# Kernel tuning notes

Measured on AMD Instinct MI355X. Metric: run time of the kernel, lower is better.

## Reference

```python
import jax, jax.numpy as jnp
import numpy as np

CUR, FULL, BS, D = 1024, 2048, 4, 1024
HN, HD = 16, 64
PREV = FULL - CUR
SCALE = 1.0 / HD ** 0.5


def rel_shift(x):
    # x: (bs, hn, cur, full) -> TXL relative shift over last two dims
    b, h, q, k = x.shape
    x = jnp.pad(x, ((0, 0), (0, 0), (0, 0), (1, 0)))  # (b,h,q,k+1)
    x = x.reshape(b, h, k + 1, q)[:, :, 1:, :]
    return x.reshape(b, h, q, k)


def setup_inputs() -> dict:
    key = jax.random.key(0)
    ks = jax.random.split(key, 16)
    s = 0.02
    inputs = jax.random.normal(ks[0], (CUR, BS, D), jnp.float32)
    pos_embedding = jax.random.normal(ks[1], (FULL, 1, D), jnp.float32)
    full_input = jax.random.normal(ks[2], (FULL, BS, D), jnp.float32)
    # causal mask: query i (absolute pos i+PREV) cannot attend to key j > i+PREV
    i = jnp.arange(CUR)[:, None]
    j = jnp.arange(FULL)[None, :]
    mask = (j > i + PREV)[:, :, None]  # (cur, full, 1) bool
    W_kv = jax.random.normal(ks[3], (D, 2 * HN * HD), jnp.float32) * s
    b_kv = jnp.zeros((2 * HN * HD,), jnp.float32)
    W_q = jax.random.normal(ks[4], (D, HN * HD), jnp.float32) * s
    b_q = jnp.zeros((HN * HD,), jnp.float32)
    W_pos = jax.random.normal(ks[5], (D, HN * HD), jnp.float32) * s
    b_pos = jnp.zeros((HN * HD,), jnp.float32)
    W_proj = jax.random.normal(ks[6], (HN * HD, D), jnp.float32) * s
    b_proj = jnp.zeros((D,), jnp.float32)
    u = jax.random.normal(ks[7], (HN, HD), jnp.float32) * s
    v = jax.random.normal(ks[8], (HN, HD), jnp.float32) * s
    return dict(inputs=inputs, pos_embedding=pos_embedding, full_input=full_input,
                u=u, v=v, mask=mask, W_kv=W_kv, b_kv=b_kv, W_q=W_q, b_q=b_q,
                W_pos=W_pos, b_pos=b_pos, W_proj=W_proj, b_proj=b_proj)


def reference(inputs, pos_embedding, full_input, u, v, mask,
              W_kv, b_kv, W_q, b_q, W_pos, b_pos, W_proj, b_proj):
    cur, bs, _ = inputs.shape
    full = full_input.shape[0]
    kv = full_input @ W_kv + b_kv                      # (full, bs, 2*hn*hd)
    k, val = jnp.split(kv, 2, axis=-1)
    k = k.reshape(full, bs, HN, HD)
    val = val.reshape(full, bs, HN, HD)
    q = (inputs @ W_q + b_q).reshape(cur, bs, HN, HD)
    r = (pos_embedding @ W_pos + b_pos).reshape(full, HN, HD)
    content = jnp.einsum('ibhd,jbhd->bhij', q + u, k)   # (bs,hn,cur,full)
    position = jnp.einsum('ibhd,jhd->bhij', q + v, r)
    position = rel_shift(position)
    attn = (content + position) * SCALE
    attn = jnp.where(mask[None, :, :, 0][:, None, :, :], -jnp.inf, attn)
    attn = jax.nn.softmax(attn, axis=-1)
    out = jnp.einsum('bhij,jbhd->ibhd', attn, val).reshape(cur, bs, HN * HD)
    return out @ W_proj + b_proj
```

## Files before the change

### kernel.cpp

```cpp
#include <hip/hip_runtime.h>


typedef _Float16 half8 __attribute__((ext_vector_type(8)));
typedef _Float16 half4v __attribute__((ext_vector_type(4)));
typedef float f32x4 __attribute__((ext_vector_type(4)));

typedef const __attribute__((address_space(1))) void* gas_ptr;
typedef __attribute__((address_space(3))) void* las_ptr;

__device__ __forceinline__ void load_lds16(const void* g, void* l) {
  __builtin_amdgcn_global_load_lds((gas_ptr)g, (las_ptr)l, 16, 0, 0);
}

__global__ __launch_bounds__(256) void prep(
    const float* __restrict__ inputs, const float* __restrict__ full_inp,
    const float* __restrict__ pos_emb, const float* __restrict__ Wq,
    const float* __restrict__ Wkv, const float* __restrict__ Wpos,
    const float* __restrict__ Wproj, _Float16* __restrict__ o_in,
    _Float16* __restrict__ o_full, _Float16* __restrict__ o_pos,
    _Float16* __restrict__ owq, _Float16* __restrict__ owkv,
    _Float16* __restrict__ owpos, _Float16* __restrict__ owproj) {
  __shared__ _Float16 tile[64][65];
  const int bx = blockIdx.x;
  const int t = threadIdx.x;
  if (bx < 2048) {
#pragma unroll
    for (int it = 0; it < 7; ++it) {
      const size_t g = (size_t)bx * 256 + t + (size_t)it * (2048 * 256);
      float4 vv;
      _Float16* dptr;
      if (g < (1u << 20)) {
        const int rd = (int)(g >> 8), b = rd >> 10, i = rd & 1023;
        const size_t sg = ((size_t)(i * 4 + b) << 8) + (g & 255);
        vv = *(const float4*)(inputs + sg * 4);
        dptr = o_in + g * 4;
      } else if (g < (3u << 20)) {
        const size_t gd = g - (1u << 20);
        const int rd = (int)(gd >> 8), b = rd >> 11, j = rd & 2047;
        const size_t sg = ((size_t)(j * 4 + b) << 8) + (gd & 255);
        vv = *(const float4*)(full_inp + sg * 4);
        dptr = o_full + gd * 4;
      } else {
        const size_t gd = g - (3u << 20);
        vv = *(const float4*)(pos_emb + gd * 4);
        dptr = o_pos + gd * 4;
      }
      half4v hh;
      hh[0] = (_Float16)vv.x; hh[1] = (_Float16)vv.y;
      hh[2] = (_Float16)vv.z; hh[3] = (_Float16)vv.w;
      *(half4v*)dptr = hh;
    }
    return;
  }
  const int wb = bx - 2048;
  const float* W;
  _Float16* Wt;
  int N, tidx;
  if (wb < 256) { W = Wq; Wt = owq; N = 1024; tidx = wb; }
  else if (wb < 768) { W = Wkv; Wt = owkv; N = 2048; tidx = wb - 256; }
  else if (wb < 1024) { W = Wpos; Wt = owpos; N = 1024; tidx = wb - 768; }
  else { W = Wproj; Wt = owproj; N = 1024; tidx = wb - 1024; }
  const int K = 1024;
  const int n0 = (tidx % (N >> 6)) * 64, k0 = (tidx / (N >> 6)) * 64;
  const int rr = t >> 2, cc = (t & 3) * 16;
#pragma unroll
  for (int i = 0; i < 4; ++i) {
    float4 v = *(const float4*)&W[(size_t)(k0 + rr) * N + n0 + cc + i * 4];
    tile[rr][cc + i * 4 + 0] = (_Float16)v.x;
    tile[rr][cc + i * 4 + 1] = (_Float16)v.y;
    tile[rr][cc + i * 4 + 2] = (_Float16)v.z;
    tile[rr][cc + i * 4 + 3] = (_Float16)v.w;
  }
  __syncthreads();
  const int n = t >> 2, kc = (t & 3) * 16;
#pragma unroll
  for (int i = 0; i < 4; ++i) {
    half4v h;
    h[0] = tile[kc + i * 4 + 0][n];
    h[1] = tile[kc + i * 4 + 1][n];
    h[2] = tile[kc + i * 4 + 2][n];
    h[3] = tile[kc + i * 4 + 3][n];
    *(half4v*)&Wt[(size_t)(n0 + n) * K + k0 + kc + i * 4] = h;
  }
}

__global__ __launch_bounds__(256, 2) void gemm3(
    const _Float16* __restrict__ Aq, const _Float16* __restrict__ Akv,
    const _Float16* __restrict__ Ar, const _Float16* __restrict__ Btq,
    const _Float16* __restrict__ Btkv, const _Float16* __restrict__ Btr,
    const float* __restrict__ bq, const float* __restrict__ bkv,
    const float* __restrict__ br, const float* __restrict__ uu,
    _Float16* __restrict__ qfu, _Float16* __restrict__ kf,
    _Float16* __restrict__ vfT, _Float16* __restrict__ rf) {
  __shared__ _Float16 smem[128 * 128];
  _Float16* As = smem;
  _Float16* Bs = smem + 8192;
  const int gb = blockIdx.x;
  const _Float16* A;
  const _Float16* Bt;
  const float* bias;
  int mode, bm, bn;
  if (gb < 256) {
    mode = 1; A = Aq; Bt = Btq; bias = bq;
    bn = (gb & 7) * 128; bm = (gb >> 3) * 128;
  } else if (gb < 1280) {
    mode = 2; A = Akv; Bt = Btkv; bias = bkv;
    const int j = gb - 256;
    bn = (j & 15) * 128; bm = (j >> 4) * 128;
  } else {
    mode = 3; A = Ar; Bt = Btr; bias = br;
    const int j = gb - 1280;
    bn = (j & 7) * 128; bm = (j >> 3) * 128;
  }
  const int K = 1024;
  const int t = threadIdx.x, w = t >> 6, l = t & 63;
  const int l15 = l & 15, l4 = l >> 4;
  const int wm = (w >> 1) * 64, wn = (w & 1) * 64;

  f32x4 acc[4][4];
  const f32x4 z4 = {0.f, 0.f, 0.f, 0.f};
#pragma unroll
  for (int i = 0; i < 4; ++i)
#pragma unroll
    for (int j = 0; j < 4; ++j) acc[i][j] = z4;

  const char* Abase = (const char*)A + (size_t)bm * K * 2;
  const char* Bbase = (const char*)Bt + (size_t)bn * K * 2;

  for (int k0 = 0; k0 < K; k0 += 64) {
    __syncthreads();
#pragma unroll
    for (int iss = 0; iss < 4; ++iss) {
      const int off = w * 4096 + iss * 1024 + l * 16;
      const int row = off >> 7;
      const int sw = ((((off >> 4) & 7) ^ (row & 7)) << 4);
      load_lds16(Abase + (size_t)row * (K * 2) + k0 * 2 + sw, (char*)As + off);
      load_lds16(Bbase + (size_t)row * (K * 2) + k0 * 2 + sw, (char*)Bs + off);
    }
    __syncthreads();
#pragma unroll
    for (int ks = 0; ks < 2; ++ks) {
      const int ch = ((ks * 4 + l4) ^ (l15 & 7)) * 8;
      half8 af[4], bf[4];
#pragma unroll
      for (int mt = 0; mt < 4; ++mt)
        af[mt] = *(const half8*)&As[(wm + mt * 16 + l15) * 64 + ch];
#pragma unroll
      for (int nt = 0; nt < 4; ++nt)
        bf[nt] = *(const half8*)&Bs[(wn + nt * 16 + l15) * 64 + ch];
#pragma unroll
      for (int mt = 0; mt < 4; ++mt)
#pragma unroll
        for (int nt = 0; nt < 4; ++nt)
          acc[mt][nt] = __builtin_amdgcn_mfma_f32_16x16x32_f16(
              af[mt], bf[nt], acc[mt][nt], 0, 0, 0);
    }
  }

  if (mode == 2 && bn >= 1024) {
    const int b = bm >> 11, j0m = bm & 2047;
    const int hbase = (bn - 1024) >> 6;
#pragma unroll
    for (int ch = 0; ch < 2; ++ch) {
      __syncthreads();
      if (((wn >> 6) & 1) == ch) {
#pragma unroll
        for (int mt = 0; mt < 4; ++mt)
#pragma unroll
          for (int r = 0; r < 4; ++r) {
            const int rowl = wm + mt * 16 + l4 * 4 + r;
#pragma unroll
            for (int nt = 0; nt < 4; ++nt) {
              const int coll = nt * 16 + l15;
              smem[rowl * 66 + coll] =
                  (_Float16)(acc[mt][nt][r] + bias[bn + wn + coll]);
            }
          }
      }
      __syncthreads();
#pragma unroll
      for (int it = 0; it < 4; ++it) {
        const int c = t + 256 * it;
        const int d = c >> 4, ck = c & 15;
        half8 v8;
#pragma unroll
        for (int z = 0; z < 8; ++z) v8[z] = smem[(ck * 8 + z) * 66 + d];
        *(half8*)&vfT[(((size_t)(b * 16 + hbase + ch) * 64 + d) << 11) + j0m +
                      ck * 8] = v8;
      }
    }
    return;
  }

#pragma unroll
  for (int mt = 0; mt < 4; ++mt)
#pragma unroll
    for (int r = 0; r < 4; ++r) {
      const int rowl = wm + mt * 16 + l4 * 4 + r;
#pragma unroll
      for (int nt = 0; nt < 4; ++nt) {
        const int col = bn + wn + nt * 16 + l15;
        const float val = acc[mt][nt][r] + bias[col];
        if (mode == 1) {
          const int b = bm >> 10, i0m = bm & 1023;
          const int h = col >> 6, d = col & 63;
          qfu[(((size_t)(b * 16 + h) * 1024 + i0m + rowl) << 6) + d] =
              (_Float16)((val + uu[col]) * 0.125f);
        } else if (mode == 2) {
          const int b = bm >> 11, j0m = bm & 2047;
          const int h = col >> 6, d = col & 63;
          kf[(((size_t)(b * 16 + h) * 2048 + j0m + rowl) << 6) + d] =
              (_Float16)val;
        } else {
          const int h = col >> 6, d = col & 63;
          rf[(((size_t)h * 2048 + bm + rowl) << 6) + d] = (_Float16)val;
        }
      }
    }
}

__global__ __launch_bounds__(256, 2) void gemm_proj(
    const _Float16* __restrict__ A, const _Float16* __restrict__ Bt,
    const float* __restrict__ bias, float* __restrict__ out0, int M, int N,
    int K) {
  __shared__ _Float16 As[128 * 64];
  __shared__ _Float16 Bs[64 * 64];
  const int t = threadIdx.x, w = t >> 6, l = t & 63;
  const int l15 = l & 15, l4 = l >> 4;
  const int bm = blockIdx.y * 128, bn = blockIdx.x * 64;
  const int wm = (w >> 1) * 64, wn = (w & 1) * 32;

  f32x4 acc[4][2];
  const f32x4 z4 = {0.f, 0.f, 0.f, 0.f};
#pragma unroll
  for (int i = 0; i < 4; ++i)
#pragma unroll
    for (int j = 0; j < 2; ++j) acc[i][j] = z4;

  const char* Abase = (const char*)A + (size_t)bm * K * 2;
  const char* Bbase = (const char*)Bt + (size_t)bn * K * 2;

  for (int k0 = 0; k0 < K; k0 += 64) {
    __syncthreads();
#pragma unroll
    for (int iss = 0; iss < 4; ++iss) {
      const int off = w * 4096 + iss * 1024 + l * 16;
      const int row = off >> 7;
      const int sw = ((((off >> 4) & 7) ^ (row & 7)) << 4);
      load_lds16(Abase + (size_t)row * (K * 2) + k0 * 2 + sw, (char*)As + off);
    }
#pragma unroll
    for (int iss = 0; iss < 2; ++iss) {
      const int off = w * 1024 + iss * 4096 + l * 16;
      const int row = off >> 7;
      const int sw = ((((off >> 4) & 7) ^ (row & 7)) << 4);
      load_lds16(Bbase + (size_t)row * (K * 2) + k0 * 2 + sw, (char*)Bs + off);
    }
    __syncthreads();
#pragma unroll
    for (int ks = 0; ks < 2; ++ks) {
      const int ch = ((ks * 4 + l4) ^ (l15 & 7)) * 8;
      half8 af[4], bf[2];
#pragma unroll
      for (int mt = 0; mt < 4; ++mt)
        af[mt] = *(const half8*)&As[(wm + mt * 16 + l15) * 64 + ch];
#pragma unroll
      for (int nt = 0; nt < 2; ++nt)
        bf[nt] = *(const half8*)&Bs[(wn + nt * 16 + l15) * 64 + ch];
#pragma unroll
      for (int mt = 0; mt < 4; ++mt)
#pragma unroll
        for (int nt = 0; nt < 2; ++nt)
          acc[mt][nt] = __builtin_amdgcn_mfma_f32_16x16x32_f16(
              af[mt], bf[nt], acc[mt][nt], 0, 0, 0);
    }
  }

#pragma unroll
  for (int mt = 0; mt < 4; ++mt)
#pragma unroll
    for (int r = 0; r < 4; ++r) {
      const int row = bm + wm + mt * 16 + l4 * 4 + r;
#pragma unroll
      for (int nt = 0; nt < 2; ++nt) {
        const int col = bn + wn + nt * 16 + l15;
        out0[(size_t)row * N + col] = acc[mt][nt][r] + bias[col];
      }
    }
}

__global__ __launch_bounds__(256, 2) void attn_mfma(
    const _Float16* __restrict__ qfu,
    const _Float16* __restrict__ kf,
    const _Float16* __restrict__ vfT,
    const _Float16* __restrict__ rf,
    const float* __restrict__ u,
    const float* __restrict__ v,
    _Float16* __restrict__ attn_out)
{
  __shared__ _Float16 ks[64 * 64];
  __shared__ _Float16 vts[64 * 64];
  __shared__ _Float16 rs[256 * 64];
  __shared__ _Float16 pA[2][4][16 * 64];

  const int t = threadIdx.x, w = t >> 6, l = t & 63;
  const int l15 = l & 15, l4 = l >> 4;
  const int id = blockIdx.x;
  const int bh = ((id >> 3) & 7) * 8 + (id & 7);
  const int qt = id >> 6;
  const int bx = (qt < 4) ? (7 - qt) : (qt - 4);
  const int i0 = bx * 128;
  const int h = bh & 15, b = bh >> 4;

  const char* kfb = (const char*)(kf + (((size_t)bh * 2048) << 6));
  const char* vg = (const char*)(vfT + (((size_t)bh) << 17));
  const char* rg = (const char*)(rf + (((size_t)h) << 17));

  half8 qa0[2], qa1[2], qv0[2], qv1[2];
  {
    half8 dl0, dl1;
#pragma unroll
    for (int z = 0; z < 8; ++z) {
      const int di = l4 * 8 + z;
      dl0[z] = (_Float16)(0.125f * (v[h * 64 + di] - u[h * 64 + di]));
      dl1[z] = (_Float16)(0.125f * (v[h * 64 + 32 + di] - u[h * 64 + 32 + di]));
    }
#pragma unroll
    for (int g = 0; g < 2; ++g) {
      const size_t qo =
          (((size_t)bh * 1024 + i0 + 64 * g + w * 16 + l15) << 6) + l4 * 8;
      qa0[g] = *(const half8*)(qfu + qo);
      qa1[g] = *(const half8*)(qfu + qo + 32);
      qv0[g] = qa0[g] + dl0;
      qv1[g] = qa1[g] + dl1;
    }
  }
  const f32x4 z4 = {0.f, 0.f, 0.f, 0.f};
  f32x4 o[2][4];
  float lsum[2][4];
#pragma unroll
  for (int g = 0; g < 2; ++g)
#pragma unroll
    for (int nt = 0; nt < 4; ++nt) { o[g][nt] = z4; lsum[g][nt] = 0.f; }

  const int mb0 = 960 - i0;
  const int njt = 2 * bx + 18;

#pragma unroll
  for (int iss = 0; iss < 6; ++iss) {
    const int off = w * 1024 + iss * 4096 + l * 16;
    const int q = off >> 7;
    const int cph = (off >> 4) & 7;
    const int slot = (mb0 - 64 + q) & 255;
    int m = mb0 - 64 + q;
    m = m < 2047 ? m : 2047;
    load_lds16(rg + (size_t)m * 128 + ((cph ^ (slot & 7)) << 4),
               (char*)rs + slot * 128 + cph * 16);
  }

  for (int jt = 0; jt < njt; ++jt) {
    const int j0 = jt * 64;
    const int m_base = j0 - i0 + 960;
    __syncthreads();
    {
      const char* kg = kfb + (size_t)j0 * 128;
#pragma unroll
      for (int iss = 0; iss < 2; ++iss) {
        const int off = w * 1024 + iss * 4096 + l * 16;
        const int row = off >> 7;
        const int cph = (off >> 4) & 7;
        const int sw = ((cph ^ (row & 7)) << 4);
        load_lds16(kg + (size_t)row * 128 + sw, (char*)ks + off);
        load_lds16(vg + (size_t)row * 4096 + (size_t)j0 * 2 + sw,
                   (char*)vts + off);
      }
    }
    if (jt > 0) {
      const int m0 = m_base + 64;
#pragma unroll
      for (int iss = 0; iss < 2; ++iss) {
        const int off = w * 1024 + iss * 4096 + l * 16;
        const int q = off >> 7;
        const int cph = (off >> 4) & 7;
        const int slot = (m0 + q) & 255;
        int m = m0 + q;
        m = m < 2047 ? m : 2047;
        load_lds16(rg + (size_t)m * 128 + ((cph ^ (slot & 7)) << 4),
                   (char*)rs + slot * 128 + cph * 16);
      }
    }
    __syncthreads();

    f32x4 sc[2][4];
    __builtin_amdgcn_s_setprio(1);
#pragma unroll
    for (int nt = 0; nt < 4; ++nt) {
      const int row = nt * 16 + l15;
      const int rsw = row & 7;
      const half8 b0 = *(const half8*)&ks[row * 64 + ((l4 ^ rsw) * 8)];
      const half8 b1 = *(const half8*)&ks[row * 64 + (((4 + l4) ^ rsw) * 8)];
#pragma unroll
      for (int g = 0; g < 2; ++g) {
        f32x4 cc = z4;
        cc = __builtin_amdgcn_mfma_f32_16x16x32_f16(qa0[g], b0, cc, 0, 0, 0);
        cc = __builtin_amdgcn_mfma_f32_16x16x32_f16(qa1[g], b1, cc, 0, 0, 0);
        sc[g][nt] = cc;
      }
    }
    __builtin_amdgcn_s_setprio(0);

#pragma unroll
    for (int g = 0; g < 2; ++g) {
      const int cw = i0 + 64 * g - j0 + 1024 + 16 * w;
      if (g == 0 && cw < -15) continue;
      const int mbg = m_base - 64 * g;
      f32x4 accP[5];
      __builtin_amdgcn_s_setprio(1);
#pragma unroll
      for (int p = 0; p < 5; ++p) {
        const int m = mbg + (3 - w + p) * 16 + l15;
        const int slot = m & 255;
        const int ssw = slot & 7;
        const half8 b0 = *(const half8*)&rs[slot * 64 + ((l4 ^ ssw) * 8)];
        const half8 b1 = *(const half8*)&rs[slot * 64 + (((4 + l4) ^ ssw) * 8)];
        f32x4 cc = z4;
        cc = __builtin_amdgcn_mfma_f32_16x16x32_f16(qv0[g], b0, cc, 0, 0, 0);
        cc = __builtin_amdgcn_mfma_f32_16x16x32_f16(qv1[g], b1, cc, 0, 0, 0);
        accP[p] = cc;
      }
      __builtin_amdgcn_s_setprio(0);
      if (cw >= 63) {
#pragma unroll
        for (int r = 0; r < 4; ++r) {
          const int thr = 4 * l4 + r;
          const int srcl = (l4 << 4) | ((15 + l15 - thr) & 15);
          float rot[5];
#pragma unroll
          for (int p = 0; p < 5; ++p) rot[p] = __shfl(accP[p][r], srcl, 64);
          float esum = 0.f;
          const int sw2 = (thr & 7) * 8;
#pragma unroll
          for (int nt = 0; nt < 4; ++nt) {
            const float pv = (l15 <= thr) ? rot[nt] : rot[nt + 1];
            const float e = __expf(sc[g][nt][r] + pv);
            esum += e;
            pA[g][w][thr * 64 + ((16 * nt + l15) ^ sw2)] = (_Float16)e;
          }
          lsum[g][r] += esum;
        }
      } else {
#pragma unroll
        for (int r = 0; r < 4; ++r) {
          const int thr = 4 * l4 + r;
          const int srcl = (l4 << 4) | ((15 + l15 - thr) & 15);
          float rot[5];
#pragma unroll
          for (int p = 0; p < 5; ++p) rot[p] = __shfl(accP[p][r], srcl, 64);
          float esum = 0.f;
          const int sw2 = (thr & 7) * 8;
#pragma unroll
          for (int nt = 0; nt < 4; ++nt) {
            const float pv = (l15 <= thr) ? rot[nt] : rot[nt + 1];
            const bool masked = (16 * nt + l15) > (cw + thr);
            const float e = masked ? 0.f : __expf(sc[g][nt][r] + pv);
            esum += e;
            pA[g][w][thr * 64 + ((16 * nt + l15) ^ sw2)] = (_Float16)e;
          }
          lsum[g][r] += esum;
        }
      }
    }

    const bool act0 = (i0 - j0 + 1024 + 16 * w) >= -15;
    __builtin_amdgcn_s_setprio(1);
#pragma unroll
    for (int kk = 0; kk < 2; ++kk) {
      const int aoff = l15 * 64 + ((kk * 32 + l4 * 8) ^ ((l15 & 7) * 8));
      half8 a81 = *(const half8*)&pA[1][w][aoff];
      half8 a80;
      if (act0) a80 = *(const half8*)&pA[0][w][aoff];
#pragma unroll
      for (int nt = 0; nt < 4; ++nt) {
        const int row = nt * 16 + l15;
        const half8 b8 =
            *(const half8*)&vts[row * 64 + ((((kk << 2) + l4) ^ (row & 7)) * 8)];
        if (act0)
          o[0][nt] =
              __builtin_amdgcn_mfma_f32_16x16x32_f16(a80, b8, o[0][nt], 0, 0, 0);
        o[1][nt] =
            __builtin_amdgcn_mfma_f32_16x16x32_f16(a81, b8, o[1][nt], 0, 0, 0);
      }
    }
    __builtin_amdgcn_s_setprio(0);
  }

#pragma unroll
  for (int g = 0; g < 2; ++g)
#pragma unroll
    for (int r = 0; r < 4; ++r) {
      float s = lsum[g][r];
      s += __shfl_xor(s, 1, 64);
      s += __shfl_xor(s, 2, 64);
      s += __shfl_xor(s, 4, 64);
      s += __shfl_xor(s, 8, 64);
      const float inv = 1.0f / s;
      const int i = i0 + 64 * g + w * 16 + l4 * 4 + r;
      const size_t base = ((size_t)i * 4 + b) * 1024 + h * 64;
#pragma unroll
      for (int nt = 0; nt < 4; ++nt)
        attn_out[base + nt * 16 + l15] = (_Float16)(o[g][nt][r] * inv);
    }
}

extern "C" void kernel_launch(void* const* d_in, const int* in_sizes, int n_in,
                              void* d_out, int out_size, void* d_ws,
                              size_t ws_size, hipStream_t stream) {
  const float* inputs   = (const float*)d_in[0];
  const float* pos_emb  = (const float*)d_in[1];
  const float* full_inp = (const float*)d_in[2];
  const float* u        = (const float*)d_in[3];
  const float* v        = (const float*)d_in[4];
  const float* W_kv   = (const float*)d_in[6];
  const float* b_kv   = (const float*)d_in[7];
  const float* W_q    = (const float*)d_in[8];
  const float* b_q    = (const float*)d_in[9];
  const float* W_pos  = (const float*)d_in[10];
  const float* b_pos  = (const float*)d_in[11];
  const float* W_proj = (const float*)d_in[12];
  const float* b_proj = (const float*)d_in[13];
  float* out = (float*)d_out;

  char* ws = (char*)d_ws;
  const size_t MB = 1024 * 1024;
  _Float16* in_q_h    = (_Float16*)(ws);
  _Float16* in_full_h = (_Float16*)(ws + 8 * MB);
  _Float16* in_pos_h  = (_Float16*)(ws + 24 * MB);
  _Float16* attn_h    = (_Float16*)(ws + 28 * MB);
  _Float16* wq_t      = (_Float16*)(ws + 36 * MB);
  _Float16* wkv_t     = (_Float16*)(ws + 38 * MB);
  _Float16* wpos_t    = (_Float16*)(ws + 42 * MB);
  _Float16* wproj_t   = (_Float16*)(ws + 44 * MB);
  _Float16* qfu       = (_Float16*)(ws + 46 * MB);
  _Float16* kf        = (_Float16*)(ws + 54 * MB);
  _Float16* vfT       = (_Float16*)(ws + 70 * MB);
  _Float16* rf        = (_Float16*)(ws + 86 * MB);

  const dim3 blk(256);
  prep<<<dim3(3328), blk, 0, stream>>>(inputs, full_inp, pos_emb, W_q, W_kv,
                                       W_pos, W_proj, in_q_h, in_full_h,
                                       in_pos_h, wq_t, wkv_t, wpos_t, wproj_t);
  gemm3<<<dim3(1408), blk, 0, stream>>>(in_q_h, in_full_h, in_pos_h, wq_t,
                                        wkv_t, wpos_t, b_q, b_kv, b_pos, u,
                                        qfu, kf, vfT, rf);
  attn_mfma<<<dim3(512), blk, 0, stream>>>(qfu, kf, vfT, rf, u, v, attn_h);
  gemm_proj<<<dim3(16, 32), blk, 0, stream>>>(attn_h, wproj_t, b_proj, out,
                                              4096, 1024, 1024);
}
```

Measured before the change: 336.2 us.

## Double-buffer LDS tiles in projection GEMMs and drop attention setprio hints

Both projection GEMM kernels now keep two LDS buffers. The next K-slice is prefetched with global_load_lds while MFMAs run on the current slice, which cuts one of the two barriers per iteration and hides global load latency behind compute. The cost is doubled LDS per block (64KB for gemm3), which could limit occupancy. Separately, the s_setprio raise/lower hints around the MFMA sections of the attention kernel are removed, which changes wave scheduling priority.

```diff
diff --git a/kernel.cpp b/kernel.cpp
--- a/kernel.cpp
+++ b/kernel.cpp
@@ -92,9 +92,7 @@
     const float* __restrict__ br, const float* __restrict__ uu,
     _Float16* __restrict__ qfu, _Float16* __restrict__ kf,
     _Float16* __restrict__ vfT, _Float16* __restrict__ rf) {
-  __shared__ _Float16 smem[128 * 128];
-  _Float16* As = smem;
-  _Float16* Bs = smem + 8192;
+  __shared__ _Float16 smem[32768];
   const int gb = blockIdx.x;
   const _Float16* A;
   const _Float16* Bt;
@@ -127,27 +125,43 @@
   const char* Abase = (const char*)A + (size_t)bm * K * 2;
   const char* Bbase = (const char*)Bt + (size_t)bn * K * 2;
 
+#pragma unroll
+  for (int iss = 0; iss < 4; ++iss) {
+    const int off = w * 4096 + iss * 1024 + l * 16;
+    const int row = off >> 7;
+    const int sw = ((((off >> 4) & 7) ^ (row & 7)) << 4);
+    load_lds16(Abase + (size_t)row * (K * 2) + sw, (char*)smem + off);
+    load_lds16(Bbase + (size_t)row * (K * 2) + sw, (char*)smem + 16384 + off);
+  }
+  __syncthreads();
+
+  int cur = 0;
   for (int k0 = 0; k0 < K; k0 += 64) {
-    __syncthreads();
-#pragma unroll
-    for (int iss = 0; iss < 4; ++iss) {
-      const int off = w * 4096 + iss * 1024 + l * 16;
-      const int row = off >> 7;
-      const int sw = ((((off >> 4) & 7) ^ (row & 7)) << 4);
-      load_lds16(Abase + (size_t)row * (K * 2) + k0 * 2 + sw, (char*)As + off);
-      load_lds16(Bbase + (size_t)row * (K * 2) + k0 * 2 + sw, (char*)Bs + off);
-    }
-    __syncthreads();
+    if (k0 + 64 < K) {
+      const int nb = cur ^ 1;
+#pragma unroll
+      for (int iss = 0; iss < 4; ++iss) {
+        const int off = w * 4096 + iss * 1024 + l * 16;
+        const int row = off >> 7;
+        const int sw = ((((off >> 4) & 7) ^ (row & 7)) << 4);
+        load_lds16(Abase + (size_t)row * (K * 2) + (k0 + 64) * 2 + sw,
+                   (char*)smem + nb * 32768 + off);
+        load_lds16(Bbase + (size_t)row * (K * 2) + (k0 + 64) * 2 + sw,
+                   (char*)smem + nb * 32768 + 16384 + off);
+      }
+    }
+    const _Float16* Asc = smem + cur * 16384;
+    const _Float16* Bsc = smem + cur * 16384 + 8192;
 #pragma unroll
     for (int ks = 0; ks < 2; ++ks) {
       const int ch = ((ks * 4 + l4) ^ (l15 & 7)) * 8;
       half8 af[4], bf[4];
 #pragma unroll
       for (int mt = 0; mt < 4; ++mt)
-        af[mt] = *(const half8*)&As[(wm + mt * 16 + l15) * 64 + ch];
+        af[mt] = *(const half8*)&Asc[(wm + mt * 16 + l15) * 64 + ch];
 #pragma unroll
       for (int nt = 0; nt < 4; ++nt)
-        bf[nt] = *(const half8*)&Bs[(wn + nt * 16 + l15) * 64 + ch];
+        bf[nt] = *(const half8*)&Bsc[(wn + nt * 16 + l15) * 64 + ch];
 #pragma unroll
       for (int mt = 0; mt < 4; ++mt)
 #pragma unroll
@@ -155,6 +169,8 @@
           acc[mt][nt] = __builtin_amdgcn_mfma_f32_16x16x32_f16(
               af[mt], bf[nt], acc[mt][nt], 0, 0, 0);
     }
+    __syncthreads();
+    cur ^= 1;
   }
 
   if (mode == 2 && bn >= 1024) {
@@ -223,8 +239,7 @@
     const _Float16* __restrict__ A, const _Float16* __restrict__ Bt,
     const float* __restrict__ bias, float* __restrict__ out0, int M, int N,
     int K) {
-  __shared__ _Float16 As[128 * 64];
-  __shared__ _Float16 Bs[64 * 64];
+  __shared__ _Float16 smem[24576];
   const int t = threadIdx.x, w = t >> 6, l = t & 63;
   const int l15 = l & 15, l4 = l >> 4;
   const int bm = blockIdx.y * 128, bn = blockIdx.x * 64;
@@ -240,33 +255,55 @@
   const char* Abase = (const char*)A + (size_t)bm * K * 2;
   const char* Bbase = (const char*)Bt + (size_t)bn * K * 2;
 
+#pragma unroll
+  for (int iss = 0; iss < 4; ++iss) {
+    const int off = w * 4096 + iss * 1024 + l * 16;
+    const int row = off >> 7;
+    const int sw = ((((off >> 4) & 7) ^ (row & 7)) << 4);
+    load_lds16(Abase + (size_t)row * (K * 2) + sw, (char*)smem + off);
+  }
+#pragma unroll
+  for (int iss = 0; iss < 2; ++iss) {
+    const int off = w * 1024 + iss * 4096 + l * 16;
+    const int row = off >> 7;
+    const int sw = ((((off >> 4) & 7) ^ (row & 7)) << 4);
+    load_lds16(Bbase + (size_t)row * (K * 2) + sw, (char*)smem + 16384 + off);
+  }
+  __syncthreads();
+
+  int cur = 0;
   for (int k0 = 0; k0 < K; k0 += 64) {
-    __syncthreads();
-#pragma unroll
-    for (int iss = 0; iss < 4; ++iss) {
-      const int off = w * 4096 + iss * 1024 + l * 16;
-      const int row = off >> 7;
-      const int sw = ((((off >> 4) & 7) ^ (row & 7)) << 4);
-      load_lds16(Abase + (size_t)row * (K * 2) + k0 * 2 + sw, (char*)As + off);
-    }
-#pragma unroll
-    for (int iss = 0; iss < 2; ++iss) {
-      const int off = w * 1024 + iss * 4096 + l * 16;
-      const int row = off >> 7;
-      const int sw = ((((off >> 4) & 7) ^ (row & 7)) << 4);
-      load_lds16(Bbase + (size_t)row * (K * 2) + k0 * 2 + sw, (char*)Bs + off);
-    }
-    __syncthreads();
+    if (k0 + 64 < K) {
+      const int nb = cur ^ 1;
+#pragma unroll
+      for (int iss = 0; iss < 4; ++iss) {
+        const int off = w * 4096 + iss * 1024 + l * 16;
+        const int row = off >> 7;
+        const int sw = ((((off >> 4) & 7) ^ (row & 7)) << 4);
+        load_lds16(Abase + (size_t)row * (K * 2) + (k0 + 64) * 2 + sw,
+                   (char*)smem + nb * 24576 + off);
+      }
+#pragma unroll
+      for (int iss = 0; iss < 2; ++iss) {
+        const int off = w * 1024 + iss * 4096 + l * 16;
+        const int row = off >> 7;
+        const int sw = ((((off >> 4) & 7) ^ (row & 7)) << 4);
+        load_lds16(Bbase + (size_t)row * (K * 2) + (k0 + 64) * 2 + sw,
+                   (char*)smem + nb * 24576 + 16384 + off);
+      }
+    }
+    const _Float16* Asc = smem + cur * 12288;
+    const _Float16* Bsc = smem + cur * 12288 + 8192;
 #pragma unroll
     for (int ks = 0; ks < 2; ++ks) {
       const int ch = ((ks * 4 + l4) ^ (l15 & 7)) * 8;
       half8 af[4], bf[2];
 #pragma unroll
       for (int mt = 0; mt < 4; ++mt)
-        af[mt] = *(const half8*)&As[(wm + mt * 16 + l15) * 64 + ch];
+        af[mt] = *(const half8*)&Asc[(wm + mt * 16 + l15) * 64 + ch];
 #pragma unroll
       for (int nt = 0; nt < 2; ++nt)
-        bf[nt] = *(const half8*)&Bs[(wn + nt * 16 + l15) * 64 + ch];
+        bf[nt] = *(const half8*)&Bsc[(wn + nt * 16 + l15) * 64 + ch];
 #pragma unroll
       for (int mt = 0; mt < 4; ++mt)
 #pragma unroll
@@ -274,6 +311,8 @@
           acc[mt][nt] = __builtin_amdgcn_mfma_f32_16x16x32_f16(
               af[mt], bf[nt], acc[mt][nt], 0, 0, 0);
     }
+    __syncthreads();
+    cur ^= 1;
   }
 
 #pragma unroll
@@ -392,7 +431,6 @@
     __syncthreads();
 
     f32x4 sc[2][4];
-    __builtin_amdgcn_s_setprio(1);
 #pragma unroll
     for (int nt = 0; nt < 4; ++nt) {
       const int row = nt * 16 + l15;
@@ -407,7 +445,6 @@
         sc[g][nt] = cc;
       }
     }
-    __builtin_amdgcn_s_setprio(0);
 
 #pragma unroll
     for (int g = 0; g < 2; ++g) {
@@ -415,7 +452,6 @@
       if (g == 0 && cw < -15) continue;
       const int mbg = m_base - 64 * g;
       f32x4 accP[5];
-      __builtin_amdgcn_s_setprio(1);
 #pragma unroll
       for (int p = 0; p < 5; ++p) {
         const int m = mbg + (3 - w + p) * 16 + l15;
@@ -428,7 +464,6 @@
         cc = __builtin_amdgcn_mfma_f32_16x16x32_f16(qv1[g], b1, cc, 0, 0, 0);
         accP[p] = cc;
       }
-      __builtin_amdgcn_s_setprio(0);
       if (cw >= 63) {
 #pragma unroll
         for (int r = 0; r < 4; ++r) {
@@ -472,7 +507,6 @@
     }
 
     const bool act0 = (i0 - j0 + 1024 + 16 * w) >= -15;
-    __builtin_amdgcn_s_setprio(1);
 #pragma unroll
     for (int kk = 0; kk < 2; ++kk) {
       const int aoff = l15 * 64 + ((kk * 32 + l4 * 8) ^ ((l15 & 7) * 8));
@@ -491,7 +525,6 @@
             __builtin_amdgcn_mfma_f32_16x16x32_f16(a81, b8, o[1][nt], 0, 0, 0);
       }
     }
-    __builtin_amdgcn_s_setprio(0);
   }
 
 #pragma unroll
```

New measurement: 327.4 us. 1.03x faster.
